# Kernel tuning notes

Measured on AMD Instinct MI355X. Metric: run time of the kernel, lower is better.

The kernel has to match this reference:

```python
import jax, jax.numpy as jnp
import numpy as np

WORLD_SIZE = 8
M = 4096
N = 4096
K_LOCAL = 1024  # full K = WORLD_SIZE * K_LOCAL = 8192


def setup_inputs() -> dict:
    key = jax.random.key(0)
    k1, k2 = jax.random.split(key)
    # Per-rank activation shard [R, M, K_local] and weight shard [R, N, K_local]
    inp = jax.random.normal(k1, (WORLD_SIZE, M, K_LOCAL), dtype=jnp.float32) * 0.02
    w = jax.random.normal(k2, (WORLD_SIZE, N, K_LOCAL), dtype=jnp.float32) * 0.02
    return {"input": inp, "weight": w}


def reference(input, weight):
    # Each rank r computes a partial GEMM: input[r] @ weight[r].T -> [M, N].
    # Reduce(-scatter) sums partials over ranks; the single einsum contracts
    # both the rank axis (the all-reduce part) and K_local (the GEMM part).
    full = jnp.einsum("rmk,rnk->mn", input, weight)  # [M, N]
    R = input.shape[0]
    # Scatter: rank r receives rows [r*M/R : (r+1)*M/R] -> stacked [R, M/R, N]
    return full.reshape(R, full.shape[0] // R, full.shape[1])
```

## Files before the change

### kernel.cpp

```cpp
#include <hip/hip_runtime.h>
#include <cstdint>
#include <cstddef>


#define M_DIM 4096
#define N_DIM 4096
#define K_DIM 8192
#define K_LOCAL 1024
#define RANKS 8

typedef __bf16 bf16x8 __attribute__((ext_vector_type(8)));
typedef float f32x4 __attribute__((ext_vector_type(4)));

__device__ __forceinline__ unsigned short f2bf(float f) {
    unsigned int u = __float_as_uint(f);
    unsigned int r = (u + 0x7fffu + ((u >> 16) & 1u)) >> 16;
    return (unsigned short)r;
}

__global__ __launch_bounds__(256) void convert_cast(
    const float* __restrict__ srcA, unsigned short* __restrict__ dstA,
    const float* __restrict__ srcB, unsigned short* __restrict__ dstB,
    int blocks_per_tensor) {
    const float* src = srcA;
    unsigned short* dst = dstA;
    int b = blockIdx.x;
    if (b >= blocks_per_tensor) { b -= blocks_per_tensor; src = srcB; dst = dstB; }
    size_t base = (size_t)b * 4096 + threadIdx.x * 4;
#pragma unroll
    for (int i = 0; i < 4; ++i) {
        size_t e = base + i * 1024;
        f32x4 v = __builtin_nontemporal_load((const f32x4*)(src + e));
        ushort4 o;
        o.x = f2bf(v.x); o.y = f2bf(v.y); o.z = f2bf(v.z); o.w = f2bf(v.w);
        *(ushort4*)(dst + e) = o;
    }
}

__device__ __forceinline__ void gll16(const unsigned short* g, unsigned short* l) {
    __builtin_amdgcn_global_load_lds(
        (const __attribute__((address_space(1))) void*)g,
        (__attribute__((address_space(3))) void*)l,
        16, 0, 0);
}

__device__ __forceinline__ int k_off(int t) {
    return ((t >> 4) << 22) | ((t & 15) << 6);
}

#define VM8 asm volatile("s_waitcnt vmcnt(8)" ::: "memory")
#define VM2 asm volatile("s_waitcnt vmcnt(2)" ::: "memory")
#define VM0 asm volatile("s_waitcnt vmcnt(0)" ::: "memory")
#define VMNONE ((void)0)
#define BAR __builtin_amdgcn_s_barrier();

#define STAGE_A(TOFF, HALF, PBUF) { \
    _Pragma("unroll") for (int j_ = 0; j_ < 2; ++j_) \
        gll16(A + (size_t)((TOFF) + (HALF) * 131072 + thrA[j_]), \
              smem + (PBUF) * 16384 + (HALF) * 8192 + ldsOff[j_]); }

#define STAGE_B(TOFF, HALF, PBUF) { \
    _Pragma("unroll") for (int j_ = 0; j_ < 2; ++j_) \
        gll16(B + (size_t)((TOFF) + (HALF) * 131072 + thrB[j_]), \
              smem + 32768 + (PBUF) * 16384 + (HALF) * 8192 + ldsOff[j_]); }

#define READ_A(DST, BASE, MOFF) { \
    _Pragma("unroll") for (int ks_ = 0; ks_ < 2; ++ks_) \
        _Pragma("unroll") for (int mm_ = 0; mm_ < 4; ++mm_) \
            DST[ks_][mm_] = *(const bf16x8*)&(BASE)[(((MOFF) + mm_) * 16 + l15) * 64 + (ks_ ? swz1 : swz0)]; }

#define READ_B(DST, BASE, NJ0) { \
    _Pragma("unroll") for (int ks_ = 0; ks_ < 2; ++ks_) \
        _Pragma("unroll") for (int nn_ = 0; nn_ < 2; ++nn_) \
            DST[ks_][nn_] = *(const bf16x8*)&(BASE)[(bRowBase + ((NJ0) + nn_) * 16 + l15) * 64 + (ks_ ? swz1 : swz0)]; }

#define QUAD(AF, BF, MI0, NJ0) { \
    __builtin_amdgcn_s_setprio(1); \
    _Pragma("unroll") for (int ks_ = 0; ks_ < 2; ++ks_) \
        _Pragma("unroll") for (int mm_ = 0; mm_ < 4; ++mm_) \
            _Pragma("unroll") for (int nn_ = 0; nn_ < 2; ++nn_) \
                acc[(MI0) + mm_][(NJ0) + nn_] = __builtin_amdgcn_mfma_f32_16x16x32_bf16( \
                    AF[ks_][mm_], BF[ks_][nn_], acc[(MI0) + mm_][(NJ0) + nn_], 0, 0, 0); \
    __builtin_amdgcn_s_setprio(0); }

#define KTILE(PBUF, KT, S3, S4, SR, VMOP) { \
    const int t2off_ = k_off((KT) + 2); \
    unsigned short* aC_ = smem + (PBUF) * 16384 + wmIdx * 8192; \
    unsigned short* bC_ = smem + 32768 + (PBUF) * 16384 + bHalfSel * 8192; \
    unsigned short* aN_ = smem + ((PBUF) ^ 1) * 16384 + wmIdx * 8192; \
    unsigned short* bN_ = smem + 32768 + ((PBUF) ^ 1) * 16384 + bHalfSel * 8192; \
     \
    READ_A(aHi, aC_, 4) \
    QUAD(aLo, bLo, 0, 0) \
    BAR \
     \
    READ_B(bHi, bC_, 2) \
    QUAD(aHi, bLo, 4, 0) \
    BAR \
     \
    if (S3) { STAGE_A(t2off_, 0, (PBUF)) } \
    QUAD(aLo, bHi, 0, 2) \
    VMOP; \
    BAR \
     \
    if (SR) { READ_A(aLo, aN_, 0) READ_B(bLo, bN_, 0) } \
    if (S4) { STAGE_A(t2off_, 1, (PBUF)) STAGE_B(t2off_, 0, (PBUF)) STAGE_B(t2off_, 1, (PBUF)) } \
    QUAD(aHi, bHi, 4, 2) \
    BAR \
}

__global__ __launch_bounds__(512, 2) void gemm_bf16_8ph(
    const unsigned short* __restrict__ A,
    const unsigned short* __restrict__ B,
    float* __restrict__ C) {
    extern __shared__ unsigned short smem[];

    const int tid = threadIdx.x;
    const int lane = tid & 63;
    const int wave = tid >> 6;
    const int wmIdx = wave >> 2;
    const int wn = wave & 3;
    const int l15 = lane & 15;
    const int l4 = lane >> 4;
    const int bHalfSel = wn >> 1;
    const int bRowBase = (wn & 1) * 64;

    const int bid = blockIdx.x;
    const int xcd = bid & 7;
    const int idx = bid >> 3;
    const int tm = (xcd >> 2) * 8 + (idx >> 2);
    const int tn = (xcd & 3) * 4 + (idx & 3);
    const int bm0 = tm * 256;
    const int bn0 = tn * 256;

    int thrA[2], thrB[2], ldsOff[2];
#pragma unroll
    for (int j = 0; j < 2; ++j) {
        int cc = j * 512 + tid;
        int row = cc >> 3;
        int col = ((cc & 7) ^ (row & 7)) * 8;
        thrA[j] = (bm0 + row) * K_LOCAL + col;
        thrB[j] = (bn0 + row) * K_LOCAL + col;
        ldsOff[j] = cc * 8;
    }

    const int swz0 = ((0 + l4) ^ (l15 & 7)) * 8;
    const int swz1 = ((4 + l4) ^ (l15 & 7)) * 8;

    bf16x8 aLo[2][4], aHi[2][4], bLo[2][2], bHi[2][2];
    f32x4 acc[8][4] = {};

    STAGE_A(0, 0, 0)
    STAGE_A(0, 1, 0)
    STAGE_B(0, 0, 0)
    STAGE_B(0, 1, 0)
    STAGE_A(64, 0, 1)
    STAGE_A(64, 1, 1)
    STAGE_B(64, 0, 1)
    STAGE_B(64, 1, 1)
    VM8;
    BAR
    {
        unsigned short* a0_ = smem + wmIdx * 8192;
        unsigned short* b0_ = smem + 32768 + bHalfSel * 8192;
        READ_A(aLo, a0_, 0)
        READ_B(bLo, b0_, 0)
    }

#pragma unroll 1
    for (int kt = 0; kt < 126; kt += 2) {
        KTILE(0, kt, 1, 1, 1, VM2)
        KTILE(1, kt + 1, 1, 1, 1, VM2)
    }
    KTILE(0, 126, 0, 0, 1, VM0)
    KTILE(1, 127, 0, 0, 0, VMNONE)

#pragma unroll
    for (int mi = 0; mi < 8; ++mi) {
        int row0 = bm0 + wmIdx * 128 + mi * 16 + l4 * 4;
#pragma unroll
        for (int nj = 0; nj < 4; ++nj) {
            int col = bn0 + wn * 64 + nj * 16 + l15;
#pragma unroll
            for (int r = 0; r < 4; ++r)
                C[(size_t)(row0 + r) * N_DIM + col] = acc[mi][nj][r];
        }
    }
}

__global__ __launch_bounds__(256) void gemm_bf16_128(
    const unsigned short* __restrict__ A,
    const unsigned short* __restrict__ B,
    float* __restrict__ C) {
    __shared__ __align__(16) unsigned short As[128 * 64];
    __shared__ __align__(16) unsigned short Bs[128 * 64];

    const int tid = threadIdx.x;
    const int lane = tid & 63;
    const int wave = tid >> 6;
    const int wm = (wave >> 1) * 64;
    const int wnn = (wave & 1) * 64;
    const int l15 = lane & 15;
    const int l4 = lane >> 4;

    const int bid = blockIdx.x;
    const int xcd = bid & 7;
    const int q = bid >> 3;
    const int st = (q >> 2) * 8 + xcd;
    const int pos = q & 3;
    const int bm0 = ((st >> 4) * 2 + (pos >> 1)) * 128;
    const int bn0 = ((st & 15) * 2 + (pos & 1)) * 128;

    const unsigned short* ga[4];
    const unsigned short* gb[4];
    int lo[4];
#pragma unroll
    for (int p = 0; p < 4; ++p) {
        int cc = p * 256 + tid;
        int row = cc >> 3;
        int cpos = cc & 7;
        int col = (cpos ^ (row & 7)) * 8;
        ga[p] = A + (size_t)(bm0 + row) * K_LOCAL + col;
        gb[p] = B + (size_t)(bn0 + row) * K_LOCAL + col;
        lo[p] = cc * 8;
    }

    const int swz0 = ((l4 + 0) ^ (l15 & 7)) * 8;
    const int swz1 = ((l4 + 4) ^ (l15 & 7)) * 8;
    const int a_row = (wm + l15) * 64;
    const int b_row = (wnn + l15) * 64;

    f32x4 acc[4][4] = {};

    for (int r = 0; r < RANKS; ++r) {
        const size_t roff = (size_t)r * (M_DIM * (size_t)K_LOCAL);
        for (int kl = 0; kl < K_LOCAL; kl += 64) {
#pragma unroll
            for (int p = 0; p < 4; ++p) {
                gll16(ga[p] + roff + kl, &As[lo[p]]);
                gll16(gb[p] + roff + kl, &Bs[lo[p]]);
            }
            __syncthreads();
#pragma unroll
            for (int ks = 0; ks < 2; ++ks) {
                const int swz = ks ? swz1 : swz0;
                bf16x8 af[4], bfr[4];
#pragma unroll
                for (int i = 0; i < 4; ++i)
                    af[i] = *(const bf16x8*)&As[a_row + i * 16 * 64 + swz];
#pragma unroll
                for (int j = 0; j < 4; ++j)
                    bfr[j] = *(const bf16x8*)&Bs[b_row + j * 16 * 64 + swz];
#pragma unroll
                for (int i = 0; i < 4; ++i)
#pragma unroll
                    for (int j = 0; j < 4; ++j)
                        acc[i][j] = __builtin_amdgcn_mfma_f32_16x16x32_bf16(
                            af[i], bfr[j], acc[i][j], 0, 0, 0);
            }
            __syncthreads();
        }
    }

#pragma unroll
    for (int i = 0; i < 4; ++i) {
        int row0 = bm0 + wm + i * 16 + l4 * 4;
#pragma unroll
        for (int j = 0; j < 4; ++j) {
            int col = bn0 + wnn + j * 16 + l15;
#pragma unroll
            for (int r = 0; r < 4; ++r)
                C[(size_t)(row0 + r) * N_DIM + col] = acc[i][j][r];
        }
    }
}

__global__ void gemm_naive(const float* __restrict__ A, const float* __restrict__ B,
                           float* __restrict__ C) {
    __shared__ float As[16][17];
    __shared__ float Bs[16][17];
    int tx = threadIdx.x, ty = threadIdx.y;
    int m = blockIdx.y * 16 + ty;
    int n0 = blockIdx.x * 16;
    float accv = 0.f;
    for (int kt = 0; kt < K_DIM; kt += 16) {
        int r = kt >> 10;
        int k = (kt & 1023) + tx;
        As[ty][tx] = A[((size_t)r * M_DIM + m) * K_LOCAL + k];
        Bs[ty][tx] = B[((size_t)r * N_DIM + (n0 + ty)) * K_LOCAL + k];
        __syncthreads();
#pragma unroll
        for (int kk = 0; kk < 16; ++kk) accv += As[ty][kk] * Bs[tx][kk];
        __syncthreads();
    }
    C[(size_t)m * N_DIM + n0 + tx] = accv;
}

extern "C" void kernel_launch(void* const* d_in, const int* in_sizes, int n_in,
                              void* d_out, int out_size, void* d_ws, size_t ws_size,
                              hipStream_t stream) {
    const float* inp = (const float*)d_in[0];
    const float* wgt = (const float*)d_in[1];
    float* out = (float*)d_out;

    const size_t elems = (size_t)M_DIM * K_DIM;
    const size_t need = 2 * elems * sizeof(unsigned short);

    if (ws_size >= need) {
        unsigned short* Abf = (unsigned short*)d_ws;
        unsigned short* Bbf = Abf + elems;
        const int bpt = (int)(elems / 4096);
        convert_cast<<<bpt * 2, 256, 0, stream>>>(inp, Abf, wgt, Bbf, bpt);

        static int dynOK = -1;
        if (dynOK < 0) {
            dynOK = (hipFuncSetAttribute((const void*)gemm_bf16_8ph,
                                         hipFuncAttributeMaxDynamicSharedMemorySize,
                                         131072) == hipSuccess)
                        ? 1
                        : 0;
        }
        if (dynOK) {
            gemm_bf16_8ph<<<256, 512, 131072, stream>>>(Abf, Bbf, out);
        } else {
            gemm_bf16_128<<<1024, 256, 0, stream>>>(Abf, Bbf, out);
        }
    } else {
        dim3 grid(N_DIM / 16, M_DIM / 16);
        dim3 block(16, 16);
        gemm_naive<<<grid, block, 0, stream>>>(inp, wgt, out);
    }
}
```

Before: 266.1 us.

## Spread global-to-LDS staging across all four phases and double-buffer lo fragments

Reworks the four-phase k-tile schedule so that each phase issues one quarter of the next-next tile's global-to-LDS loads, instead of bunching three of them into the last phase. The lo A/B register fragments are double-buffered (aLo/aLo2, bLo/bLo2), so reads of the next tile's LDS data can start in phases three and four, overlapping the remaining MFMAs. The vmcnt wait is relaxed from 2 to 4 to match the new issue pattern, and a barrier is added before the main loop. The cost is extra VGPRs under a 512-thread, 2-blocks-per-CU bound, which risks spills. Issuing staging writes into the current buffer earlier may also race with reads other waves are still making from it.

Measured after the change: 392.6 us. 47.5% more time.

```diff
diff --git a/kernel.cpp b/kernel.cpp
--- a/kernel.cpp
+++ b/kernel.cpp
@@ -49,7 +49,7 @@
 }
 
 #define VM8 asm volatile("s_waitcnt vmcnt(8)" ::: "memory")
-#define VM2 asm volatile("s_waitcnt vmcnt(2)" ::: "memory")
+#define VM4 asm volatile("s_waitcnt vmcnt(4)" ::: "memory")
 #define VM0 asm volatile("s_waitcnt vmcnt(0)" ::: "memory")
 #define VMNONE ((void)0)
 #define BAR __builtin_amdgcn_s_barrier();
@@ -83,7 +83,7 @@
                     AF[ks_][mm_], BF[ks_][nn_], acc[(MI0) + mm_][(NJ0) + nn_], 0, 0, 0); \
     __builtin_amdgcn_s_setprio(0); }
 
-#define KTILE(PBUF, KT, S3, S4, SR, VMOP) { \
+#define KTILE(PBUF, KT, S, SR, VMOP, ALO_C, BLO_C, ALO_N, BLO_N) { \
     const int t2off_ = k_off((KT) + 2); \
     unsigned short* aC_ = smem + (PBUF) * 16384 + wmIdx * 8192; \
     unsigned short* bC_ = smem + 32768 + (PBUF) * 16384 + bHalfSel * 8192; \
@@ -91,20 +91,23 @@
     unsigned short* bN_ = smem + 32768 + ((PBUF) ^ 1) * 16384 + bHalfSel * 8192; \
      \
     READ_A(aHi, aC_, 4) \
-    QUAD(aLo, bLo, 0, 0) \
+    if (S) { STAGE_A(t2off_, 0, (PBUF)) } \
+    QUAD(ALO_C, BLO_C, 0, 0) \
     BAR \
      \
     READ_B(bHi, bC_, 2) \
-    QUAD(aHi, bLo, 4, 0) \
-    BAR \
-     \
-    if (S3) { STAGE_A(t2off_, 0, (PBUF)) } \
-    QUAD(aLo, bHi, 0, 2) \
+    if (S) { STAGE_B(t2off_, 0, (PBUF)) } \
+    QUAD(aHi, BLO_C, 4, 0) \
     VMOP; \
     BAR \
      \
-    if (SR) { READ_A(aLo, aN_, 0) READ_B(bLo, bN_, 0) } \
-    if (S4) { STAGE_A(t2off_, 1, (PBUF)) STAGE_B(t2off_, 0, (PBUF)) STAGE_B(t2off_, 1, (PBUF)) } \
+    if (SR) { READ_A(ALO_N, aN_, 0) } \
+    if (S) { STAGE_A(t2off_, 1, (PBUF)) } \
+    QUAD(ALO_C, bHi, 0, 2) \
+    BAR \
+     \
+    if (SR) { READ_B(BLO_N, bN_, 0) } \
+    if (S) { STAGE_B(t2off_, 1, (PBUF)) } \
     QUAD(aHi, bHi, 4, 2) \
     BAR \
 }
@@ -147,7 +150,7 @@
     const int swz0 = ((0 + l4) ^ (l15 & 7)) * 8;
     const int swz1 = ((4 + l4) ^ (l15 & 7)) * 8;
 
-    bf16x8 aLo[2][4], aHi[2][4], bLo[2][2], bHi[2][2];
+    bf16x8 aLo[2][4], aLo2[2][4], aHi[2][4], bLo[2][2], bLo2[2][2], bHi[2][2];
     f32x4 acc[8][4] = {};
 
     STAGE_A(0, 0, 0)
@@ -166,14 +169,15 @@
         READ_A(aLo, a0_, 0)
         READ_B(bLo, b0_, 0)
     }
+    BAR
 
 #pragma unroll 1
     for (int kt = 0; kt < 126; kt += 2) {
-        KTILE(0, kt, 1, 1, 1, VM2)
-        KTILE(1, kt + 1, 1, 1, 1, VM2)
-    }
-    KTILE(0, 126, 0, 0, 1, VM0)
-    KTILE(1, 127, 0, 0, 0, VMNONE)
+        KTILE(0, kt, 1, 1, VM4, aLo, bLo, aLo2, bLo2)
+        KTILE(1, kt + 1, 1, 1, VM4, aLo2, bLo2, aLo, bLo)
+    }
+    KTILE(0, 126, 0, 1, VM0, aLo, bLo, aLo2, bLo2)
+    KTILE(1, 127, 0, 0, VMNONE, aLo2, bLo2, aLo, bLo)
 
 #pragma unroll
     for (int mi = 0; mi < 8; ++mi) {
```
